# Performance work log

Hardware: AMD Instinct MI355X
Metric: run time of the kernel (lower is better)

The kernel has to match this reference:

```python
import jax, jax.numpy as jnp
import numpy as np
from jax import lax

# Dims: B queries, N nodes, E edges (inverse edges already included), D hidden,
# R2 = 2*num_relation, T tail candidates, M text-embedded nodes, L layers.
B, N, E, D, R2, T, M, L = 4, 50000, 1600000, 64, 1000, 32, 10000, 3
NODE_RATIO, DEG_RATIO = 0.1, 1.0
K = int(NODE_RATIO * N)              # nodes kept per layer (variadic_topks on node scores)
ESEL = int(DEG_RATIO * K * E / N)    # edges kept per layer


def setup_inputs():
    key = jax.random.key(0)
    ks = jax.random.split(key, 16)
    f32 = jnp.float32
    return {
        "h_index": jax.random.randint(ks[0], (B,), 0, N),
        "r_index": jax.random.randint(ks[1], (B,), 0, R2),
        "t_index": jax.random.randint(ks[2], (B, T), 0, N),
        "all_index": jax.random.randint(ks[3], (M,), 0, N),
        "edge_src": jax.random.randint(ks[4], (E,), 0, N),
        "edge_dst": jax.random.randint(ks[5], (E,), 0, N),
        "edge_type": jax.random.randint(ks[6], (E,), 0, R2),
        "hidden_states": jax.random.normal(ks[7], (B, D), f32),
        "score_text_embs": jax.random.normal(ks[8], (M, D), f32),
        "rel_table": 0.02 * jax.random.normal(ks[9], (R2, D), f32),
        "linear_w": jax.random.normal(ks[10], (2 * D, D), f32) / np.sqrt(2 * D),
        "linear_b": jnp.zeros((D,), f32),
        "mlp_w1": jax.random.normal(ks[11], (D, 2 * D), f32) / np.sqrt(D),
        "mlp_b1": jnp.zeros((2 * D,), f32),
        "mlp_w2": jax.random.normal(ks[12], (2 * D, 1), f32) / np.sqrt(2 * D),
        "mlp_b2": jnp.zeros((1,), f32),
        "relw": 0.1 * jax.random.normal(ks[13], (L, R2, D), f32),
        "pna_w": jax.random.normal(ks[14], (L, 12 * D, D), f32) / np.sqrt(12 * D),
        "pna_b": jnp.zeros((L, D), f32),
    }


def _forward(h_index, r_index, t_index, all_index, edge_src, edge_dst, edge_type,
             hidden_states, score_text_embs, rel_table, linear_w, linear_b,
             mlp_w1, mlp_b1, mlp_w2, mlp_b2, relw, pna_w, pna_b):
    def score_fn(hidden, rel):  # hidden [n, D], rel [D] -> [n]
        rel_b = jnp.broadcast_to(rel, hidden.shape)
        heur = jnp.concatenate([hidden, rel_b], -1) @ linear_w + linear_b
        x = hidden * heur
        h1 = jax.nn.relu(x @ mlp_w1 + mlp_b1)
        return jnp.squeeze(h1 @ mlp_w2 + mlp_b2, -1)

    # pna_degree_mean = mean(log(degree_out + 1)) over the base graph
    deg_out_full = jax.ops.segment_sum(jnp.ones((E,), jnp.float32), edge_src, num_segments=N)
    dmean = jnp.mean(jnp.log(deg_out_full + 1.0))

    rel_embeds = rel_table[r_index]  # [B, D]

    def per_batch(rel, h_idx, head_emb, t_idx):
        # init_input_embeds: text embeddings at all_index, head embedding at h_idx
        hidden = (jnp.zeros((N, D), jnp.float32)
                  .at[all_index].set(score_text_embs)
                  .at[h_idx].set(head_emb))
        base = score_fn(jnp.zeros((1, D), jnp.float32), rel)[0]
        score = jnp.full((N,), base, jnp.float32).at[h_idx].set(score_fn(head_emb[None], rel)[0])

        for l in range(L):
            # ---- select_edges: top-K nodes by score, then top-ESEL outgoing edges by dst score
            _, nidx = lax.top_k(score, K)
            sel = jnp.zeros((N,), bool).at[nidx].set(True)
            escore = jnp.where(sel[edge_src], score[edge_dst], -jnp.inf)
            ev, eidx = lax.top_k(escore, ESEL)
            valid = jnp.isfinite(ev)
            s, d, et = edge_src[eidx], edge_dst[eidx], edge_type[eidx]

            # ---- gated message passing on the selected subgraph (PNA aggregation)
            gate = jax.nn.sigmoid(score)
            msg = (gate[s, None] * hidden[s]) * relw[l][et]        # [ESEL, D]
            msg0 = jnp.where(valid[:, None], msg, 0.0)
            deg = jax.ops.segment_sum(valid.astype(jnp.float32), d, num_segments=N)
            sm = jax.ops.segment_sum(msg0, d, num_segments=N)
            sq = jax.ops.segment_sum(msg0 * msg0, d, num_segments=N)
            mx = jax.ops.segment_max(jnp.where(valid[:, None], msg, -jnp.inf), d, num_segments=N)
            mn = jax.ops.segment_min(jnp.where(valid[:, None], msg, jnp.inf), d, num_segments=N)
            has = (deg > 0.0)[:, None]
            degc = jnp.maximum(deg, 1.0)[:, None]
            mean = sm / degc
            std = jnp.where(has, jnp.sqrt(jax.nn.relu(sq / degc - mean * mean) + 1e-6), 0.0)
            mx = jnp.where(has, mx, 0.0)
            mn = jnp.where(has, mn, 0.0)
            logd = jnp.log(deg + 1.0)[:, None]
            amp = logd / dmean
            att = jnp.where(has, dmean / jnp.maximum(logd, 1e-6), 0.0)
            one = jnp.ones_like(amp)
            # 4 aggregators x 3 degree scalers -> [N, 12D]
            feats = jnp.concatenate([a * sc for a in (mean, mx, mn, std) for sc in (one, amp, att)], -1)
            out = feats @ pna_w[l] + pna_b[l]

            # scatter back: only nodes with subgraph out-degree > 0 are updated
            hidden = jnp.where(has, hidden + out, hidden)
            score = jnp.where(deg > 0.0, score_fn(hidden, rel), score)
        return score[t_idx]

    return jax.vmap(per_batch)(rel_embeds, h_index, hidden_states, t_index)  # [B, T]


def reference(h_index, r_index, t_index, all_index, edge_src, edge_dst, edge_type,
              hidden_states, score_text_embs, rel_table, linear_w, linear_b,
              mlp_w1, mlp_b1, mlp_w2, mlp_b2, relw, pna_w, pna_b):
    return _forward(h_index, r_index, t_index, all_index, edge_src, edge_dst, edge_type,
                    hidden_states, score_text_embs, rel_table, linear_w, linear_b,
                    mlp_w1, mlp_b1, mlp_w2, mlp_b2, relw, pna_w, pna_b)
```

## Files before the change

kernel.cpp:

```cpp
#include <hip/hip_runtime.h>
#include <cstdint>
#include <cstddef>


#define NN   50000
#define NEG  1600000
#define NR2  1000
#define NTC  32
#define NMI  10000
#define KSEL 5000u
#define ESEL 160000u
#define KEY_NEG_INF 0x007FFFFFu

#define OFF_ST    0
#define OFF_RELB  64
#define OFF_BC    128
#define OFF_BC2   2176
#define OFF_HISTA 4224
#define OFF_HISTB 69760
#define OFF_SCORE 135296
#define OFF_NSEL  185296
#define OFF_DCNT  235296
#define OFF_ROWS  285296
#define OFF_CURS  335296
#define OFF_ACT   385296
#define OFF_HID   435296
#define OFF_SRCH  3635296
#define OFF_ELIST 3955296
#define OFF_CSR   4115296
#define SBLK      4275296

#define RL(x,k) __int_as_float(__builtin_amdgcn_readlane(__float_as_int(x),(k)))
#define BBASE unsigned* B = WB + (size_t)blockIdx.y * (size_t)sb

__device__ inline unsigned fkey(float f){
  unsigned u = __float_as_uint(f);
  if ((u << 1) == 0u) u = 0u;
  return (u & 0x80000000u) ? ~u : (u | 0x80000000u);
}

__device__ inline float waveSumF(float v){
  #pragma unroll
  for (int d = 1; d < 64; d <<= 1) v += __shfl_xor(v, d);
  return v;
}

__device__ inline void ldsHashAdd(unsigned* hkey, unsigned* hval, unsigned bin, unsigned cnt){
  unsigned h = (bin * 2654435761u) >> 23;
  while (true){
    unsigned prev = atomicCAS(hkey + h, 0xFFFFFFFFu, bin);
    if (prev == 0xFFFFFFFFu || prev == bin){ atomicAdd(hval + h, cnt); return; }
    h = (h + 1u) & 511u;
  }
}


__global__ void k_lastm(const int* __restrict__ all_index, int* __restrict__ lastm){
  int i = blockIdx.x * 256 + threadIdx.x;
  if (i < NMI) atomicMax(lastm + all_index[i], i);
}

__global__ void k_degfull(const int* __restrict__ esrc, unsigned* __restrict__ degf){
  int i = blockIdx.x * 256 + threadIdx.x;
  if (i < NEG) atomicAdd(degf + esrc[i], 1u);
}

__global__ void k_dsum(const unsigned* __restrict__ degf, float* __restrict__ gstF){
  int i = blockIdx.x * 256 + threadIdx.x;
  float v = (i < NN) ? logf((float)degf[i] + 1.f) : 0.f;
  v = waveSumF(v);
  if ((threadIdx.x & 63) == 0) atomicAdd(gstF + 4, v);
}

__global__ void k_finalize(float* __restrict__ gstF, const float* __restrict__ b1,
                           const float* __restrict__ w2, const float* __restrict__ b2){
  gstF[5] = gstF[4] / (float)NN;
  float s = 0.f;
  for (int m = 0; m < 128; m++) s += fmaxf(b1[m], 0.f) * w2[m];
  gstF[6] = s + b2[0];
}


__global__ void k_relb(unsigned* WB, long sb, int b0,
                       const int* __restrict__ r_index, const float* __restrict__ hs,
                       const float* __restrict__ rel_table, const float* __restrict__ lw,
                       const float* __restrict__ lb, const float* __restrict__ w1,
                       const float* __restrict__ b1, const float* __restrict__ w2,
                       const float* __restrict__ b2){
  BBASE;
  float* relb = (float*)(B + OFF_RELB);
  float* stF  = (float*)(B + OFF_ST);
  int b = b0 + blockIdx.y;
  int j = threadIdx.x;
  int r = r_index[b];
  float acc = lb[j];
  for (int k = 0; k < 64; k++) acc = fmaf(rel_table[(size_t)r*64 + k], lw[(64 + k)*64 + j], acc);
  relb[j] = acc;
  float heur = acc;
  for (int k = 0; k < 64; k++) heur = fmaf(hs[b*64 + k], lw[k*64 + j], heur);
  float x = hs[b*64 + j] * heur;
  float o = 0.f;
  for (int half = 0; half < 2; half++){
    float a = b1[half*64 + j];
    for (int k = 0; k < 64; k++) a = fmaf(__shfl(x, k), w1[k*128 + half*64 + j], a);
    o = fmaf(fmaxf(a, 0.f), w2[half*64 + j], o);
  }
  o = waveSumF(o);
  if (j == 0) stF[7] = o + b2[0];
}

__global__ void k_inithidden(unsigned* WB, long sb, int b0,
                             const int* __restrict__ lastm, const float* __restrict__ ste,
                             const float* __restrict__ hs, const int* __restrict__ h_index){
  BBASE;
  float4* hidden = (float4*)(B + OFF_HID);
  const float4* ste4 = (const float4*)ste;
  const float4* hs4  = (const float4*)hs;
  int b = b0 + blockIdx.y;
  int idx = blockIdx.x * 256 + threadIdx.x;
  int n = idx >> 4, j = idx & 15;
  int h = h_index[b];
  float4 v = make_float4(0.f, 0.f, 0.f, 0.f);
  int lm = lastm[n];
  if (lm >= 0) v = ste4[(size_t)lm*16 + j];
  if (n == h)  v = hs4[b*16 + j];
  hidden[idx] = v;
}

__global__ void k_initscore(unsigned* WB, long sb, int b0,
                            const int* __restrict__ h_index, const float* __restrict__ gstF){
  BBASE;
  float* score = (float*)(B + OFF_SCORE);
  unsigned* st = B + OFF_ST;
  float* stF = (float*)st;
  int b = b0 + blockIdx.y;
  int i = blockIdx.x * 256 + threadIdx.x;
  if (i < NN) score[i] = (i == h_index[b]) ? stF[7] : gstF[6];
  if (i == 0){ st[0] = 0u; st[1] = KSEL; }
}


__global__ __launch_bounds__(256) void k_hist(unsigned* WB, long sb, int pass){
  BBASE;
  const unsigned* st = B + OFF_ST;
  const float* score = (const float*)(B + OFF_SCORE);
  unsigned* hist = B + ((pass == 1) ? OFF_HISTA : OFF_HISTB);
  __shared__ unsigned hkey[512];
  __shared__ unsigned hval[512];
  for (int t = threadIdx.x; t < 512; t += 256){ hkey[t] = 0xFFFFFFFFu; hval[t] = 0u; }
  __syncthreads();
  int i = blockIdx.x * 256 + threadIdx.x;
  unsigned bin = 0xFFFFFFFFu;
  if (i < NN){
    unsigned k = fkey(score[i]);
    if (pass == 1) bin = k >> 16;
    else if ((k >> 16) == (st[0] >> 16)) bin = k & 0xFFFFu;
  }
  bool active = (bin != 0xFFFFFFFFu);
  int lane = threadIdx.x & 63;
  #pragma unroll
  for (int r = 0; r < 2; r++){
    unsigned long long mask = __ballot((int)active);
    if (mask != 0ull){
      int leader = __ffsll(mask) - 1;
      unsigned lbin = (unsigned)__shfl((int)bin, leader);
      bool same = active && (bin == lbin);
      unsigned long long smask = __ballot((int)same);
      if (lane == leader) ldsHashAdd(hkey, hval, lbin, (unsigned)__popcll(smask));
      if (same) active = false;
    }
  }
  if (active) ldsHashAdd(hkey, hval, bin, 1u);
  __syncthreads();
  for (int t = threadIdx.x; t < 512; t += 256){
    unsigned vv = hval[t];
    if (vv) atomicAdd(hist + hkey[t], vv);
  }
}

__global__ void k_indegW(unsigned* WB, long sb,
                         const int* __restrict__ esrc, const int* __restrict__ edst){
  BBASE;
  unsigned* st = B + OFF_ST;
  const unsigned* nsel = B + OFF_NSEL;
  unsigned* indeg = B + OFF_CURS;
  int i = blockIdx.x * 256 + threadIdx.x;
  if (i < NEG && nsel[esrc[i]]) atomicAdd(indeg + edst[i], 1u);
  if (i == 0){ st[0] = 0u; st[1] = ESEL; st[2] = 0u; st[3] = 0u; st[4] = 0u; st[5] = 0u; }
}

__global__ __launch_bounds__(256) void k_histW(unsigned* WB, long sb, int pass){
  BBASE;
  const unsigned* st = B + OFF_ST;
  const unsigned* indeg = B + OFF_CURS;
  const float* score = (const float*)(B + OFF_SCORE);
  unsigned* hist = B + ((pass == 1) ? OFF_HISTA : OFF_HISTB);
  __shared__ unsigned hkey[512];
  __shared__ unsigned hval[512];
  for (int t = threadIdx.x; t < 512; t += 256){ hkey[t] = 0xFFFFFFFFu; hval[t] = 0u; }
  __syncthreads();
  int i = blockIdx.x * 256 + threadIdx.x;
  unsigned w = (i < NN) ? indeg[i] : 0u;
  if (w){
    unsigned k = fkey(score[i]);
    unsigned bin = 0xFFFFFFFFu;
    if (pass == 1) bin = k >> 16;
    else if ((k >> 16) == (st[0] >> 16)) bin = k & 0xFFFFu;
    if (bin != 0xFFFFFFFFu) ldsHashAdd(hkey, hval, bin, w);
  }
  __syncthreads();
  for (int t = threadIdx.x; t < 512; t += 256){
    unsigned vv = hval[t];
    if (vv) atomicAdd(hist + hkey[t], vv);
  }
}

__global__ __launch_bounds__(1024) void k_pick16(unsigned* WB, long sb, int pass){
  BBASE;
  unsigned* st = B + OFF_ST;
  const unsigned* hist = B + ((pass == 1) ? OFF_HISTA : OFF_HISTB);
  __shared__ unsigned csum[1024];
  __shared__ unsigned sc[1024];
  int t = threadIdx.x;
  unsigned R = st[1];
  unsigned s = 0;
  {
    const unsigned* hp = hist + (unsigned)t * 64u;
    for (int b = 0; b < 64; b++) s += hp[b];
  }
  csum[t] = s; sc[t] = s; __syncthreads();
  for (int d = 1; d < 1024; d <<= 1){
    unsigned v = (t >= d) ? sc[t - d] : 0u;
    __syncthreads();
    sc[t] += v;
    __syncthreads();
  }
  unsigned total = sc[1023];
  unsigned above = total - sc[t];
  unsigned cs = csum[t];
  if (above < R && above + cs >= R){
    unsigned cum = above;
    for (int b = 63; b >= 0; b--){
      unsigned c = hist[(unsigned)(t*64 + b)];
      if (cum + c >= R){
        unsigned bstar = (unsigned)(t*64 + b);
        if (pass == 1) st[0] = bstar << 16; else st[0] = st[0] | bstar;
        st[1] = R - cum;
        break;
      }
      cum += c;
    }
  }
  if (t == 0 && total < R){
    if (pass == 1) st[0] = KEY_NEG_INF & 0xFFFF0000u;
    else           st[0] = st[0] | 0xFFFFu;
    st[1] = R - total;
  }
}

__global__ __launch_bounds__(1024) void k_countEq(unsigned* WB, long sb, int mode, int n,
                                                  const int* __restrict__ esrc,
                                                  const int* __restrict__ edst){
  BBASE;
  unsigned* hz = B + OFF_HISTA;
  for (unsigned j = blockIdx.x * 1024u + threadIdx.x; j < 131072u; j += gridDim.x * 1024u)
    hz[j] = 0u;
  unsigned* dcnt = B + OFF_DCNT;
  const unsigned* st = B + OFF_ST;
  const unsigned* nsel = B + OFF_NSEL;
  const float* score = (const float*)(B + OFF_SCORE);
  unsigned* bcE = B + OFF_BC;
  unsigned* bcG = B + OFF_BC2;
  int i = blockIdx.x * 1024 + threadIdx.x;
  if (i < NN) dcnt[i] = 0u;
  unsigned v = st[0];
  unsigned k = 0u;
  if (i < n){
    if (mode) k = nsel[esrc[i]] ? fkey(score[edst[i]]) : KEY_NEG_INF;
    else      k = fkey(score[i]);
  }
  bool eq = (i < n) && (k == v);
  bool gt = (i < n) && (k > v);
  unsigned long long ebal = __ballot((int)eq);
  unsigned long long gbal = __ballot((int)gt);
  __shared__ unsigned wshE[16];
  __shared__ unsigned wshG[16];
  int wid = threadIdx.x >> 6, lane = threadIdx.x & 63;
  if (lane == 0){ wshE[wid] = (unsigned)__popcll(ebal); wshG[wid] = (unsigned)__popcll(gbal); }
  __syncthreads();
  if (threadIdx.x == 0){
    unsigned te = 0, tg = 0;
    for (int w = 0; w < 16; w++){ te += wshE[w]; tg += wshG[w]; }
    bcE[blockIdx.x] = te; bcG[blockIdx.x] = tg;
  }
}

__global__ __launch_bounds__(1024) void k_scanBlocks(unsigned* WB, long sb, int nbk){
  BBASE;
  unsigned* blockcnt = B + OFF_BC;
  __shared__ unsigned sc[2048];
  int t = threadIdx.x;
  unsigned a  = (t < nbk) ? blockcnt[t] : 0u;
  unsigned b2 = (1024 + t < nbk) ? blockcnt[1024 + t] : 0u;
  sc[t] = a; sc[1024 + t] = b2; __syncthreads();
  for (int d = 1; d < 2048; d <<= 1){
    unsigned v1 = (t >= d) ? sc[t - d] : 0u;
    unsigned v2 = (1024 + t >= d) ? sc[1024 + t - d] : 0u;
    __syncthreads();
    sc[t] += v1; sc[1024 + t] += v2;
    __syncthreads();
  }
  if (t < nbk) blockcnt[t] = sc[t] - a;
  if (1024 + t < nbk) blockcnt[1024 + t] = sc[1024 + t] - b2;
}

__global__ __launch_bounds__(1024) void k_scanBlocks2(unsigned* WB, long sb, int nbk){
  BBASE;
  unsigned* st = B + OFF_ST;
  unsigned* bcE = B + OFF_BC;
  unsigned* bcG = B + OFF_BC2;
  __shared__ unsigned se[2048];
  __shared__ unsigned sg[2048];
  int t = threadIdx.x;
  unsigned e0 = (t < nbk) ? bcE[t] : 0u;
  unsigned e1 = (1024 + t < nbk) ? bcE[1024 + t] : 0u;
  unsigned g0 = (t < nbk) ? bcG[t] : 0u;
  unsigned g1 = (1024 + t < nbk) ? bcG[1024 + t] : 0u;
  se[t] = e0; se[1024 + t] = e1; sg[t] = g0; sg[1024 + t] = g1;
  __syncthreads();
  for (int d = 1; d < 2048; d <<= 1){
    unsigned a1 = (t >= d) ? se[t - d] : 0u;
    unsigned a2 = (1024 + t >= d) ? se[1024 + t - d] : 0u;
    unsigned c1 = (t >= d) ? sg[t - d] : 0u;
    unsigned c2 = (1024 + t >= d) ? sg[1024 + t - d] : 0u;
    __syncthreads();
    se[t] += a1; se[1024 + t] += a2; sg[t] += c1; sg[1024 + t] += c2;
    __syncthreads();
  }
  if (t < nbk) bcE[t] = se[t] - e0;
  if (1024 + t < nbk) bcE[1024 + t] = se[1024 + t] - e1;
  if (t < nbk) bcG[t] = sg[t] - g0;
  if (1024 + t < nbk) bcG[1024 + t] = sg[1024 + t] - g1;
  if (t == 0){
    unsigned gtTot = sg[2047];
    st[4] = gtTot;
    st[2] = gtTot + ((st[0] > KEY_NEG_INF) ? st[1] : 0u);
  }
}

__global__ __launch_bounds__(1024) void k_selNodes(unsigned* WB, long sb){
  BBASE;
  const unsigned* st = B + OFF_ST;
  const unsigned* blockcnt = B + OFF_BC;
  const float* score = (const float*)(B + OFF_SCORE);
  unsigned* nsel = B + OFF_NSEL;
  unsigned* curs = B + OFF_CURS;
  int i = blockIdx.x * 1024 + threadIdx.x;
  if (i < NN) curs[i] = 0u;
  unsigned v = st[0], R = st[1];
  unsigned k = (i < NN) ? fkey(score[i]) : 0u;
  bool eq = (i < NN) && (k == v);
  unsigned long long bal = __ballot((int)eq);
  __shared__ unsigned wsh[16];
  int wid = threadIdx.x >> 6, lane = threadIdx.x & 63;
  if (lane == 0) wsh[wid] = (unsigned)__popcll(bal);
  __syncthreads();
  unsigned woff = 0;
  for (int w = 0; w < wid; w++) woff += wsh[w];
  unsigned lpre = (unsigned)__popcll(bal & ((1ull << lane) - 1ull));
  unsigned rank = blockcnt[blockIdx.x] + woff + lpre;
  if (i < NN) nsel[i] = (k > v || (eq && rank < R)) ? 1u : 0u;
}

__global__ __launch_bounds__(1024) void k_selEdgesCompact(unsigned* WB, long sb,
                                                          const int* __restrict__ esrc,
                                                          const int* __restrict__ edst){
  BBASE;
  const unsigned* st = B + OFF_ST;
  const unsigned* bcE = B + OFF_BC;
  const unsigned* bcG = B + OFF_BC2;
  const unsigned* nsel = B + OFF_NSEL;
  const float* score = (const float*)(B + OFF_SCORE);
  unsigned* elist = B + OFF_ELIST;
  unsigned* dcnt = B + OFF_DCNT;
  int i = blockIdx.x * 1024 + threadIdx.x;
  unsigned v = st[0], R = st[1], gtTot = st[4];
  unsigned k = 0u;
  if (i < NEG) k = nsel[esrc[i]] ? fkey(score[edst[i]]) : KEY_NEG_INF;
  bool eq = (i < NEG) && (k == v);
  bool gt = (i < NEG) && (k > v);
  unsigned long long ebal = __ballot((int)eq);
  unsigned long long gbal = __ballot((int)gt);
  __shared__ unsigned wshE[16];
  __shared__ unsigned wshG[16];
  int wid = threadIdx.x >> 6, lane = threadIdx.x & 63;
  if (lane == 0){ wshE[wid] = (unsigned)__popcll(ebal); wshG[wid] = (unsigned)__popcll(gbal); }
  __syncthreads();
  unsigned eoff = 0, goff = 0;
  for (int w = 0; w < 16 && w < wid; w++){ eoff += wshE[w]; goff += wshG[w]; }
  unsigned long long ltm = (1ull << lane) - 1ull;
  if (gt){
    elist[bcG[blockIdx.x] + goff + (unsigned)__popcll(gbal & ltm)] = (unsigned)i;
    atomicAdd(dcnt + edst[i], 1u);
  }
  if (eq){
    unsigned rank = bcE[blockIdx.x] + eoff + (unsigned)__popcll(ebal & ltm);
    if (v > KEY_NEG_INF && rank < R){
      elist[gtTot + rank] = (unsigned)i;
      atomicAdd(dcnt + edst[i], 1u);
    }
  }
}


__global__ __launch_bounds__(1024) void k_blocksumsInt(unsigned* WB, long sb){
  BBASE;
  const unsigned* dcnt = B + OFF_DCNT;
  unsigned* blockcnt = B + OFF_BC;
  int i = blockIdx.x * 1024 + threadIdx.x;
  unsigned v = (i < NN) ? dcnt[i] : 0u;
  #pragma unroll
  for (int d = 1; d < 64; d <<= 1) v += (unsigned)__shfl_xor((int)v, d);
  __shared__ unsigned wsh[16];
  int wid = threadIdx.x >> 6, lane = threadIdx.x & 63;
  if (lane == 0) wsh[wid] = v;
  __syncthreads();
  if (threadIdx.x == 0){
    unsigned tot = 0;
    for (int w = 0; w < 16; w++) tot += wsh[w];
    blockcnt[blockIdx.x] = tot;
  }
}

__global__ __launch_bounds__(1024) void k_rowSnap(unsigned* WB, long sb){
  BBASE;
  unsigned* st = B + OFF_ST;
  const unsigned* dcnt = B + OFF_DCNT;
  const unsigned* blockcnt = B + OFF_BC;
  unsigned* rowstart = B + OFF_ROWS;
  unsigned* curs = B + OFF_CURS;
  unsigned* actl = B + OFF_ACT;
  unsigned* srcmap = B + OFF_NSEL;
  const float* score = (const float*)(B + OFF_SCORE);
  const float* hidden = (const float*)(B + OFF_HID);
  float* srch = (float*)(B + OFF_SRCH);
  int i = blockIdx.x * 1024 + threadIdx.x;
  int wid = threadIdx.x >> 6, lane = threadIdx.x & 63;
  unsigned d = (i < NN) ? dcnt[i] : 0u;
  unsigned v = d;
  #pragma unroll
  for (int dl = 1; dl < 64; dl <<= 1){
    unsigned t2 = (unsigned)__shfl_up((int)v, dl);
    if (lane >= dl) v += t2;
  }
  bool act = (i < NN) && (d > 0u);
  unsigned long long abal = __ballot((int)act);
  __shared__ unsigned wsh[16];
  __shared__ unsigned awsh[16];
  __shared__ unsigned abase;
  if (lane == 63) wsh[wid] = v;
  if (lane == 0) awsh[wid] = (unsigned)__popcll(abal);
  __syncthreads();
  if (threadIdx.x == 0){
    unsigned tot = 0;
    for (int w = 0; w < 16; w++) tot += awsh[w];
    abase = atomicAdd(st + 3, tot);
  }
  unsigned woff = 0, aoff = 0;
  for (int w = 0; w < wid; w++){ woff += wsh[w]; aoff += awsh[w]; }
  __syncthreads();
  unsigned excl = blockcnt[blockIdx.x] + woff + (v - d);
  if (i < NN){ rowstart[i] = excl; curs[i] = excl; }
  if (act) actl[abase + aoff + (unsigned)__popcll(abal & ((1ull << lane) - 1ull))] = (unsigned)i;

  int base = i - lane;
  if (base >= NN) return;
  bool sel = (i < NN) && (srcmap[i] != 0u);
  unsigned long long bal = __ballot((int)sel);
  if (bal == 0ull) return;
  unsigned slotbase = 0;
  if (lane == 0) slotbase = atomicAdd(st + 5, (unsigned)__popcll(bal));
  slotbase = (unsigned)__shfl((int)slotbase, 0);
  unsigned long long m2 = bal;
  unsigned idx = 0;
  while (m2){
    int j = __ffsll(m2) - 1;
    m2 = m2 - (m2 bitand (0ull - m2));
    int node = base + j;
    unsigned slot = slotbase + idx; idx++;
    if (lane == 0) srcmap[node] = slot;
    float g = 1.f / (1.f + expf(-score[node]));
    srch[(size_t)slot*64 + lane] = g * hidden[(size_t)node*64 + lane];
  }
}

__global__ void k_scatter(unsigned* WB, long sb, const int* __restrict__ esrc,
                          const int* __restrict__ edst, const int* __restrict__ etype){
  BBASE;
  const unsigned* st = B + OFF_ST;
  const unsigned* elist = B + OFF_ELIST;
  const unsigned* srcmap = B + OFF_NSEL;
  unsigned* curs = B + OFF_CURS;
  unsigned* csr = B + OFF_CSR;
  unsigned i = blockIdx.x * 256 + threadIdx.x;
  if (i < st[2]){
    unsigned e = elist[i];
    unsigned slot = srcmap[esrc[e]];
    unsigned pk = (slot << 10) | (unsigned)etype[e];
    unsigned pos = atomicAdd(curs + edst[e], 1u);
    csr[pos] = pk;
  }
}


__global__ __launch_bounds__(256) void k_aggpna(unsigned* WB, long sb,
    const float* __restrict__ relw, const float* __restrict__ pw,
    const float* __restrict__ pb, const float* __restrict__ gstF, int l){
  BBASE;
  const unsigned* st = B + OFF_ST;
  const unsigned* actl = B + OFF_ACT;
  const unsigned* dcnt = B + OFF_DCNT;
  const unsigned* rows = B + OFF_ROWS;
  const unsigned* csr = B + OFF_CSR;
  const float* srch = (const float*)(B + OFF_SRCH);
  float* hidden = (float*)(B + OFF_HID);
  const float* relw_l = relw + (size_t)l * NR2 * 64;
  const float* pw_l = pw + (size_t)l * 768 * 64;

  __shared__ float aggL[2 * 64 * 64];

  int lane = threadIdx.x & 63;
  int w = threadIdx.x >> 6;
  unsigned nact = st[3];
  unsigned nbase = (unsigned)blockIdx.x * 64u;
  float dmean = gstF[5];

  unsigned slotM = nbase + (unsigned)lane;
  int nodeM = (slotM < nact) ? (int)actl[slotM] : -1;
  float dvM = (nodeM >= 0) ? (float)dcnt[nodeM] : 0.f;
  float logd = logf(dvM + 1.f);
  float ampv = logd / dmean;
  float attv = dmean / fmaxf(logd, 1e-6f);
  int jbase = __builtin_amdgcn_readfirstlane((int)(threadIdx.x >> 6)) * 16;
  float acc[16];
  #pragma unroll
  for (int jj = 0; jj < 16; jj++) acc[jj] = pb[(size_t)l*64 + jbase + jj];

  float mnS[16], sdS[16];
  #pragma unroll
  for (int i = 0; i < 16; i++){
    int nloc = w * 16 + i;
    unsigned slot = nbase + (unsigned)nloc;
    float pmean = 0.f, pmax = 0.f;
    mnS[i] = 0.f; sdS[i] = 0.f;
    if (slot < nact){
      int node = (int)actl[slot];
      unsigned cnt = dcnt[node], rs = rows[node];
      float sm_ = 0.f, sq_ = 0.f;
      float mx_ = -__builtin_huge_valf(), mn_ = __builtin_huge_valf();
      for (unsigned ii = 0; ii < cnt; ii += 4u){
        unsigned i1 = (ii + 1u < cnt) ? ii + 1u : ii;
        unsigned i2 = (ii + 2u < cnt) ? ii + 2u : ii;
        unsigned i3 = (ii + 3u < cnt) ? ii + 3u : ii;
        unsigned pk0 = csr[rs + ii];
        unsigned pk1 = csr[rs + i1];
        unsigned pk2 = csr[rs + i2];
        unsigned pk3 = csr[rs + i3];
        float s0 = srch[(size_t)(pk0 >> 10)*64 + lane];
        float r0 = relw_l[(size_t)(pk0 & 1023u)*64 + lane];
        float s1 = srch[(size_t)(pk1 >> 10)*64 + lane];
        float r1 = relw_l[(size_t)(pk1 & 1023u)*64 + lane];
        float s2 = srch[(size_t)(pk2 >> 10)*64 + lane];
        float r2 = relw_l[(size_t)(pk2 & 1023u)*64 + lane];
        float s3 = srch[(size_t)(pk3 >> 10)*64 + lane];
        float r3 = relw_l[(size_t)(pk3 & 1023u)*64 + lane];
        float m = s0 * r0;
        sm_ += m; sq_ = fmaf(m, m, sq_); mx_ = fmaxf(mx_, m); mn_ = fminf(mn_, m);
        if (ii + 1u < cnt){
          m = s1 * r1;
          sm_ += m; sq_ = fmaf(m, m, sq_); mx_ = fmaxf(mx_, m); mn_ = fminf(mn_, m);
        }
        if (ii + 2u < cnt){
          m = s2 * r2;
          sm_ += m; sq_ = fmaf(m, m, sq_); mx_ = fmaxf(mx_, m); mn_ = fminf(mn_, m);
        }
        if (ii + 3u < cnt){
          m = s3 * r3;
          sm_ += m; sq_ = fmaf(m, m, sq_); mx_ = fmaxf(mx_, m); mn_ = fminf(mn_, m);
        }
      }
      float dv = (float)cnt;
      float degc = fmaxf(dv, 1.f);
      float me = sm_ / degc;
      pmean = me;
      pmax = mx_;
      mnS[i] = mn_;
      sdS[i] = sqrtf(fmaxf(sq_ / degc - me*me, 0.f) + 1e-6f);
    }
    int col = nloc ^ lane;
    aggL[0*4096 + lane*64 + col] = pmean;
    aggL[1*4096 + lane*64 + col] = pmax;
  }

  for (int half = 0; half < 2; half++){
    if (half){
      __syncthreads();
      #pragma unroll
      for (int i = 0; i < 16; i++){
        int nloc = w * 16 + i;
        int col = nloc ^ lane;
        aggL[0*4096 + lane*64 + col] = mnS[i];
        aggL[1*4096 + lane*64 + col] = sdS[i];
      }
    }
    __syncthreads();
    for (int cc = 0; cc < 6; cc++){
      int c = half*6 + cc;
      int s = cc - (cc/3)*3;
      float sc = (s == 0) ? 1.f : ((s == 1) ? ampv : attv);
      const float* wc = pw_l + (size_t)c*64*64 + jbase;
      int abase = (cc / 3) * 4096;
      #pragma unroll 4
      for (int k = 0; k < 64; k++){
        float fv = aggL[abase + k*64 + (lane ^ k)] * sc;
        const float* wp = wc + (size_t)k*64;
        #pragma unroll
        for (int jj = 0; jj < 16; jj++)
          acc[jj] = fmaf(fv, wp[jj], acc[jj]);
      }
    }
  }
  if (nodeM >= 0){
    float* hp = hidden + (size_t)nodeM*64 + jbase;
    #pragma unroll
    for (int q = 0; q < 4; q++){
      float4 h = *(float4*)(hp + q*4);
      h.x += acc[q*4+0]; h.y += acc[q*4+1]; h.z += acc[q*4+2]; h.w += acc[q*4+3];
      *(float4*)(hp + q*4) = h;
    }
  }
}


__global__ __launch_bounds__(256) void k_scoreK(unsigned* WB, long sb,
    const float* __restrict__ lw, const float* __restrict__ w1,
    const float* __restrict__ b1, const float* __restrict__ w2,
    const float* __restrict__ b2){
  BBASE;
  unsigned* st = B + OFF_ST;
  if (blockIdx.x == 0 && threadIdx.x == 0){ st[0] = 0u; st[1] = KSEL; }
  const unsigned* actl = B + OFF_ACT;
  const float* hidden = (const float*)(B + OFF_HID);
  const float* relb = (const float*)(B + OFF_RELB);
  float* score = (float*)(B + OFF_SCORE);
  unsigned nact = st[3];
  int wv = (blockIdx.x * 256 + threadIdx.x) >> 6;
  int lane = threadIdx.x & 63;
  unsigned slot0 = (unsigned)wv * 8u;
  if (slot0 >= nact) return;
  int node[8];
  #pragma unroll
  for (int n = 0; n < 8; n++){
    unsigned s = slot0 + (unsigned)n;
    node[n] = (s < nact) ? (int)actl[s] : -1;
  }
  float wreg[64];
  #pragma unroll
  for (int k = 0; k < 64; k++) wreg[k] = lw[k*64 + lane];
  float relbv = relb[lane];
  float hidv[8];
  #pragma unroll
  for (int n = 0; n < 8; n++)
    hidv[n] = (node[n] >= 0) ? hidden[(size_t)node[n]*64 + lane] : 0.f;
  float hv[8];
  #pragma unroll
  for (int n = 0; n < 8; n++) hv[n] = relbv;
  #pragma unroll
  for (int k = 0; k < 64; k++){
    float w = wreg[k];
    #pragma unroll
    for (int n = 0; n < 8; n++) hv[n] = fmaf(RL(hidv[n], k), w, hv[n]);
  }
  float xv[8];
  #pragma unroll
  for (int n = 0; n < 8; n++) xv[n] = hidv[n] * hv[n];
  float outv[8];
  #pragma unroll
  for (int n = 0; n < 8; n++) outv[n] = 0.f;
  for (int half = 0; half < 2; half++){
    #pragma unroll
    for (int k = 0; k < 64; k++) wreg[k] = w1[k*128 + half*64 + lane];
    float a[8];
    float b1l = b1[half*64 + lane];
    #pragma unroll
    for (int n = 0; n < 8; n++) a[n] = b1l;
    #pragma unroll
    for (int k = 0; k < 64; k++){
      float w = wreg[k];
      #pragma unroll
      for (int n = 0; n < 8; n++) a[n] = fmaf(RL(xv[n], k), w, a[n]);
    }
    float w2l = w2[half*64 + lane];
    #pragma unroll
    for (int n = 0; n < 8; n++) outv[n] = fmaf(fmaxf(a[n], 0.f), w2l, outv[n]);
  }
  float b2v = b2[0];
  #pragma unroll
  for (int n = 0; n < 8; n++){
    float r = waveSumF(outv[n]);
    if (lane == 0 && node[n] >= 0) score[node[n]] = r + b2v;
  }
}

__global__ void k_out(unsigned* WB, long sb, int b0,
                      const int* __restrict__ t_index, float* __restrict__ out){
  BBASE;
  const float* score = (const float*)(B + OFF_SCORE);
  int b = b0 + blockIdx.y;
  int t = threadIdx.x;
  if (t < NTC) out[b*NTC + t] = score[t_index[b*NTC + t]];
}


extern "C" void kernel_launch(void* const* d_in, const int* in_sizes, int n_in,
                              void* d_out, int out_size, void* d_ws, size_t ws_size,
                              hipStream_t stream){
  (void)in_sizes; (void)n_in; (void)out_size;
  const int*   h_index  = (const int*)d_in[0];
  const int*   r_index  = (const int*)d_in[1];
  const int*   t_index  = (const int*)d_in[2];
  const int*   all_idx  = (const int*)d_in[3];
  const int*   esrc     = (const int*)d_in[4];
  const int*   edst     = (const int*)d_in[5];
  const int*   etype    = (const int*)d_in[6];
  const float* hs       = (const float*)d_in[7];
  const float* ste      = (const float*)d_in[8];
  const float* rel_tab  = (const float*)d_in[9];
  const float* lw       = (const float*)d_in[10];
  const float* lb       = (const float*)d_in[11];
  const float* w1       = (const float*)d_in[12];
  const float* b1       = (const float*)d_in[13];
  const float* w2       = (const float*)d_in[14];
  const float* b2       = (const float*)d_in[15];
  const float* relw     = (const float*)d_in[16];
  const float* pna_w    = (const float*)d_in[17];
  const float* pna_b    = (const float*)d_in[18];
  float* out = (float*)d_out;

  unsigned* W = (unsigned*)d_ws;
  int*      LASTM = (int*)W;
  unsigned* DEGF  = W + 50000;
  float*    GSTF  = (float*)(W + 100000);
  unsigned* WB    = W + 100064;

  size_t needB = (size_t)(100064 + 4*(size_t)SBLK) * 4u;
  int nb; long sb; int nseq;
  if (ws_size >= needB){ nb = 4; sb = SBLK; nseq = 1; }
  else                 { nb = 1; sb = 0;    nseq = 4; }

  (void)hipMemsetAsync(W + 100000, 0, 64 * 4, stream);
  (void)hipMemsetAsync(LASTM, 0xFF, NN * 4, stream);
  (void)hipMemsetAsync(DEGF, 0, NN * 4, stream);
  for (int q = 0; q < nb; q++)
    (void)hipMemsetAsync(WB + (size_t)q*SBLK + OFF_HISTA, 0, 131072 * 4, stream);

  const int GB_E256  = (NEG + 255) / 256;
  const int GB_N256  = (NN + 255) / 256;
  const int GB_N1024 = (NN + 1023) / 1024;
  const int GB_E1024 = (NEG + 1023) / 1024;
  const int GB_H4    = (NN * 16) / 256;
  const int GB_A2    = (NN + 63) / 64;
  const int GB_A     = 1563;
  const int GB_ES    = (int)(ESEL / 256);

  k_lastm<<<(NMI + 255) / 256, 256, 0, stream>>>(all_idx, LASTM);
  k_degfull<<<GB_E256, 256, 0, stream>>>(esrc, DEGF);
  k_dsum<<<GB_N256, 256, 0, stream>>>(DEGF, GSTF);
  k_finalize<<<1, 1, 0, stream>>>(GSTF, b1, w2, b2);

  for (int q = 0; q < nseq; q++){
    int b0 = (nb == 4) ? 0 : q;
    k_relb<<<dim3(1, nb), 64, 0, stream>>>(WB, sb, b0, r_index, hs, rel_tab, lw, lb, w1, b1, w2, b2);
    k_inithidden<<<dim3(GB_H4, nb), 256, 0, stream>>>(WB, sb, b0, LASTM, ste, hs, h_index);
    k_initscore<<<dim3(GB_N256, nb), 256, 0, stream>>>(WB, sb, b0, h_index, GSTF);

    for (int l = 0; l < 3; l++){
      k_hist<<<dim3(GB_N256, nb), 256, 0, stream>>>(WB, sb, 1);
      k_pick16<<<dim3(1, nb), 1024, 0, stream>>>(WB, sb, 1);
      k_hist<<<dim3(GB_N256, nb), 256, 0, stream>>>(WB, sb, 0);
      k_pick16<<<dim3(1, nb), 1024, 0, stream>>>(WB, sb, 0);
      k_countEq<<<dim3(GB_N1024, nb), 1024, 0, stream>>>(WB, sb, 0, NN, esrc, edst);
      k_scanBlocks<<<dim3(1, nb), 1024, 0, stream>>>(WB, sb, GB_N1024);
      k_selNodes<<<dim3(GB_N1024, nb), 1024, 0, stream>>>(WB, sb);
      k_indegW<<<dim3(GB_E256, nb), 256, 0, stream>>>(WB, sb, esrc, edst);
      k_histW<<<dim3(GB_N256, nb), 256, 0, stream>>>(WB, sb, 1);
      k_pick16<<<dim3(1, nb), 1024, 0, stream>>>(WB, sb, 1);
      k_histW<<<dim3(GB_N256, nb), 256, 0, stream>>>(WB, sb, 0);
      k_pick16<<<dim3(1, nb), 1024, 0, stream>>>(WB, sb, 0);
      k_countEq<<<dim3(GB_E1024, nb), 1024, 0, stream>>>(WB, sb, 1, NEG, esrc, edst);
      k_scanBlocks2<<<dim3(1, nb), 1024, 0, stream>>>(WB, sb, GB_E1024);
      k_selEdgesCompact<<<dim3(GB_E1024, nb), 1024, 0, stream>>>(WB, sb, esrc, edst);
      k_blocksumsInt<<<dim3(GB_N1024, nb), 1024, 0, stream>>>(WB, sb);
      k_scanBlocks<<<dim3(1, nb), 1024, 0, stream>>>(WB, sb, GB_N1024);
      k_rowSnap<<<dim3(GB_N1024, nb), 1024, 0, stream>>>(WB, sb);
      k_scatter<<<dim3(GB_ES, nb), 256, 0, stream>>>(WB, sb, esrc, edst, etype);
      k_aggpna<<<dim3(GB_A2, nb), 256, 0, stream>>>(WB, sb, relw, pna_w, pna_b, GSTF, l);
      k_scoreK<<<dim3(GB_A, nb), 256, 0, stream>>>(WB, sb, lw, w1, b1, w2, b2);
    }
    k_out<<<dim3(1, nb), 32, 0, stream>>>(WB, sb, b0, t_index, out);
  }
}
```

Before: 2.634 ms.

## Restructure score MLP kernel to stage node tiles in LDS with uniform weight loads

The per-node score MLP now processes 64 active nodes per block. Hidden vectors are staged transposed into swizzled shared memory so each lane owns a node and each wave computes a 16-wide slice of output features, with weights read as wave-uniform loads. This replaces the per-wave readlane broadcasts and the per-lane weight register arrays, which are meant to be the main cost. In exchange it adds shared memory, three block barriers and a final transpose-and-reduce pass.

```diff
diff --git a/kernel.cpp b/kernel.cpp
--- a/kernel.cpp
+++ b/kernel.cpp
@@ -653,62 +653,77 @@
   const float* hidden = (const float*)(B + OFF_HID);
   const float* relb = (const float*)(B + OFF_RELB);
   float* score = (float*)(B + OFF_SCORE);
+
+  __shared__ float P0[64 * 64];
+  __shared__ float P1[64 * 64];
+
+  int lane = threadIdx.x & 63;
+  int w = threadIdx.x >> 6;
   unsigned nact = st[3];
-  int wv = (blockIdx.x * 256 + threadIdx.x) >> 6;
-  int lane = threadIdx.x & 63;
-  unsigned slot0 = (unsigned)wv * 8u;
-  if (slot0 >= nact) return;
-  int node[8];
-  #pragma unroll
-  for (int n = 0; n < 8; n++){
-    unsigned s = slot0 + (unsigned)n;
-    node[n] = (s < nact) ? (int)actl[s] : -1;
-  }
-  float wreg[64];
-  #pragma unroll
-  for (int k = 0; k < 64; k++) wreg[k] = lw[k*64 + lane];
-  float relbv = relb[lane];
-  float hidv[8];
-  #pragma unroll
-  for (int n = 0; n < 8; n++)
-    hidv[n] = (node[n] >= 0) ? hidden[(size_t)node[n]*64 + lane] : 0.f;
-  float hv[8];
-  #pragma unroll
-  for (int n = 0; n < 8; n++) hv[n] = relbv;
-  #pragma unroll
+  unsigned nbase = (unsigned)blockIdx.x * 64u;
+  if (nbase >= nact) return;
+
+  #pragma unroll
+  for (int i = 0; i < 16; i++){
+    int nloc = w * 16 + i;
+    unsigned slot = nbase + (unsigned)nloc;
+    float hv = 0.f;
+    if (slot < nact){
+      int node = (int)actl[slot];
+      hv = hidden[(size_t)node*64 + lane];
+    }
+    P0[lane*64 + (nloc ^ lane)] = hv;
+  }
+  __syncthreads();
+
+  int jb = __builtin_amdgcn_readfirstlane(w) * 16;
+  float heur[16];
+  #pragma unroll
+  for (int i = 0; i < 16; i++) heur[i] = relb[jb + i];
+  #pragma unroll 4
   for (int k = 0; k < 64; k++){
-    float w = wreg[k];
+    float hk = P0[k*64 + (lane ^ k)];
+    const float* lwk = lw + k*64 + jb;
     #pragma unroll
-    for (int n = 0; n < 8; n++) hv[n] = fmaf(RL(hidv[n], k), w, hv[n]);
-  }
-  float xv[8];
-  #pragma unroll
-  for (int n = 0; n < 8; n++) xv[n] = hidv[n] * hv[n];
-  float outv[8];
-  #pragma unroll
-  for (int n = 0; n < 8; n++) outv[n] = 0.f;
-  for (int half = 0; half < 2; half++){
+    for (int i = 0; i < 16; i++) heur[i] = fmaf(hk, lwk[i], heur[i]);
+  }
+  #pragma unroll
+  for (int i = 0; i < 16; i++){
+    int j = jb + i;
+    float hj = P0[j*64 + (lane ^ j)];
+    P1[j*64 + (lane ^ j)] = hj * heur[i];
+  }
+  __syncthreads();
+
+  float alo[16], ahi[16];
+  #pragma unroll
+  for (int mm = 0; mm < 16; mm++){ alo[mm] = b1[jb + mm]; ahi[mm] = b1[64 + jb + mm]; }
+  #pragma unroll 4
+  for (int j = 0; j < 64; j++){
+    float xj = P1[j*64 + (lane ^ j)];
+    const float* w1j = w1 + j*128;
     #pragma unroll
-    for (int k = 0; k < 64; k++) wreg[k] = w1[k*128 + half*64 + lane];
-    float a[8];
-    float b1l = b1[half*64 + lane];
-    #pragma unroll
-    for (int n = 0; n < 8; n++) a[n] = b1l;
-    #pragma unroll
-    for (int k = 0; k < 64; k++){
-      float w = wreg[k];
-      #pragma unroll
-      for (int n = 0; n < 8; n++) a[n] = fmaf(RL(xv[n], k), w, a[n]);
-    }
-    float w2l = w2[half*64 + lane];
-    #pragma unroll
-    for (int n = 0; n < 8; n++) outv[n] = fmaf(fmaxf(a[n], 0.f), w2l, outv[n]);
-  }
+    for (int mm = 0; mm < 16; mm++){
+      alo[mm] = fmaf(xj, w1j[jb + mm], alo[mm]);
+      ahi[mm] = fmaf(xj, w1j[64 + jb + mm], ahi[mm]);
+    }
+  }
+  #pragma unroll
+  for (int mm = 0; mm < 16; mm++){
+    int j = jb + mm;
+    float p = fmaf(fmaxf(alo[mm], 0.f), w2[j], 0.f);
+    p = fmaf(fmaxf(ahi[mm], 0.f), w2[64 + j], p);
+    P0[j*64 + (lane ^ j)] = p;
+  }
+  __syncthreads();
+
   float b2v = b2[0];
-  #pragma unroll
-  for (int n = 0; n < 8; n++){
-    float r = waveSumF(outv[n]);
-    if (lane == 0 && node[n] >= 0) score[node[n]] = r + b2v;
+  for (int i = 0; i < 16; i++){
+    int nloc = w * 16 + i;
+    unsigned slot = nbase + (unsigned)nloc;
+    float p = P0[lane*64 + (nloc ^ lane)];
+    float r = waveSumF(p);
+    if (lane == 0 && slot < nact) score[(int)actl[slot]] = r + b2v;
   }
 }
 
@@ -770,7 +785,6 @@
   const int GB_E1024 = (NEG + 1023) / 1024;
   const int GB_H4    = (NN * 16) / 256;
   const int GB_A2    = (NN + 63) / 64;
-  const int GB_A     = 1563;
   const int GB_ES    = (int)(ESEL / 256);
 
   k_lastm<<<(NMI + 255) / 256, 256, 0, stream>>>(all_idx, LASTM);
@@ -805,7 +819,7 @@
       k_rowSnap<<<dim3(GB_N1024, nb), 1024, 0, stream>>>(WB, sb);
       k_scatter<<<dim3(GB_ES, nb), 256, 0, stream>>>(WB, sb, esrc, edst, etype);
       k_aggpna<<<dim3(GB_A2, nb), 256, 0, stream>>>(WB, sb, relw, pna_w, pna_b, GSTF, l);
-      k_scoreK<<<dim3(GB_A, nb), 256, 0, stream>>>(WB, sb, lw, w1, b1, w2, b2);
+      k_scoreK<<<dim3(GB_A2, nb), 256, 0, stream>>>(WB, sb, lw, w1, b1, w2, b2);
     }
     k_out<<<dim3(1, nb), 32, 0, stream>>>(WB, sb, b0, t_index, out);
   }
```

Result: faster. 2.480 ms (-5.9%).
